# Kernel optimization log

Measured on AMD Instinct MI355X. Metric: run time of the kernel, lower is better.

The kernel has to match this reference:

```python
import jax, jax.numpy as jnp
import numpy as np
import math

D_DIM = 512
N_HEAD = 8
HIDDEN = 2048
N_LAYERS = 4
CONTEXT = 64
MAX_LEN = 5000


def make_pe(d_model, max_len=MAX_LEN):
    position = np.arange(max_len)[:, None].astype(np.float32)
    div_term = np.exp(np.arange(0, d_model, 2).astype(np.float32) * (-math.log(10000.0) / d_model))
    pe = np.zeros((max_len, d_model), dtype=np.float32)
    pe[:, 0::2] = np.sin(position * div_term)
    pe[:, 1::2] = np.cos(position * div_term)
    return jnp.asarray(pe)


def setup_inputs() -> dict:
    key = jax.random.key(0)
    ks = jax.random.split(key, 64)
    B, T, IN = 16, 2048, 512
    inp = {}
    inp["trajectory"] = jax.random.normal(ks[0], (B, T, IN), dtype=jnp.float32)
    inp["obs_length"] = jax.random.randint(ks[1], (B,), 0, T)
    s = 0.02
    inp["w_in"] = jax.random.normal(ks[2], (IN, D_DIM), dtype=jnp.float32) * s
    inp["b_in"] = jnp.zeros((D_DIM,), dtype=jnp.float32)
    # per-layer params
    params = []
    ki = 3
    for l in range(N_LAYERS):
        p = {}
        p["w_qkv"] = jax.random.normal(ks[ki], (D_DIM, 3 * D_DIM), dtype=jnp.float32) * s; ki += 1
        p["b_qkv"] = jnp.zeros((3 * D_DIM,), dtype=jnp.float32)
        p["w_o"] = jax.random.normal(ks[ki], (D_DIM, D_DIM), dtype=jnp.float32) * s; ki += 1
        p["b_o"] = jnp.zeros((D_DIM,), dtype=jnp.float32)
        p["w_ff1"] = jax.random.normal(ks[ki], (D_DIM, HIDDEN), dtype=jnp.float32) * s; ki += 1
        p["b_ff1"] = jnp.zeros((HIDDEN,), dtype=jnp.float32)
        p["w_ff2"] = jax.random.normal(ks[ki], (HIDDEN, D_DIM), dtype=jnp.float32) * s; ki += 1
        p["b_ff2"] = jnp.zeros((D_DIM,), dtype=jnp.float32)
        p["ln1_g"] = jnp.ones((D_DIM,), dtype=jnp.float32)
        p["ln1_b"] = jnp.zeros((D_DIM,), dtype=jnp.float32)
        p["ln2_g"] = jnp.ones((D_DIM,), dtype=jnp.float32)
        p["ln2_b"] = jnp.zeros((D_DIM,), dtype=jnp.float32)
        for name, v in p.items():
            inp[f"L{l}_{name}"] = v
    return inp


def layer_norm(x, g, b, eps=1e-5):
    mu = jnp.mean(x, axis=-1, keepdims=True)
    var = jnp.mean((x - mu) ** 2, axis=-1, keepdims=True)
    return (x - mu) * jax.lax.rsqrt(var + eps) * g + b


def build_attn_mask(T, obs_length, context_length):
    # boolean mask, True = masked out. Causal + per-sample context window.
    i = jnp.arange(T)[:, None]
    j = jnp.arange(T)[None, :]
    causal = j > i  # (T, T)
    # window restriction applies for rows i with context_length < i < obs_length:
    # mask positions j <= i - context_length - 1, i.e. j < i - context_length
    window = j < (i - context_length)  # (T,T)
    row_active = (i[None, :, :] > context_length) & (i[None, :, :] < obs_length[:, None, None])  # (B,T,1)
    mask = causal[None] | (window[None] & row_active)  # (B,T,T)
    return mask


def encoder_layer(x, mask_add, pad_bool, p):
    B, T, D = x.shape
    H = N_HEAD
    Dh = D // H
    qkv = x @ p["w_qkv"] + p["b_qkv"]  # (B,T,3D)
    q, k, v = jnp.split(qkv, 3, axis=-1)
    q = q.reshape(B, T, H, Dh).transpose(0, 2, 1, 3)
    k = k.reshape(B, T, H, Dh).transpose(0, 2, 1, 3)
    v = v.reshape(B, T, H, Dh).transpose(0, 2, 1, 3)
    scores = jnp.einsum("bhqd,bhkd->bhqk", q, k) / jnp.sqrt(jnp.float32(Dh))
    scores = scores + mask_add[:, None] + pad_bool[:, None, None, :] * jnp.float32(-1e9)
    attn = jax.nn.softmax(scores, axis=-1)
    ctx = jnp.einsum("bhqk,bhkd->bhqd", attn, v)
    ctx = ctx.transpose(0, 2, 1, 3).reshape(B, T, D)
    attn_out = ctx @ p["w_o"] + p["b_o"]
    x = layer_norm(x + attn_out, p["ln1_g"], p["ln1_b"])
    ff = jax.nn.relu(x @ p["w_ff1"] + p["b_ff1"]) @ p["w_ff2"] + p["b_ff2"]
    x = layer_norm(x + ff, p["ln2_g"], p["ln2_b"])
    return x


def reference(trajectory, obs_length, w_in, b_in,
              L0_w_qkv, L0_b_qkv, L0_w_o, L0_b_o, L0_w_ff1, L0_b_ff1, L0_w_ff2, L0_b_ff2, L0_ln1_g, L0_ln1_b, L0_ln2_g, L0_ln2_b,
              L1_w_qkv, L1_b_qkv, L1_w_o, L1_b_o, L1_w_ff1, L1_b_ff1, L1_w_ff2, L1_b_ff2, L1_ln1_g, L1_ln1_b, L1_ln2_g, L1_ln2_b,
              L2_w_qkv, L2_b_qkv, L2_w_o, L2_b_o, L2_w_ff1, L2_b_ff1, L2_w_ff2, L2_b_ff2, L2_ln1_g, L2_ln1_b, L2_ln2_g, L2_ln2_b,
              L3_w_qkv, L3_b_qkv, L3_w_o, L3_b_o, L3_w_ff1, L3_b_ff1, L3_w_ff2, L3_b_ff2, L3_ln1_g, L3_ln1_b, L3_ln2_g, L3_ln2_b):
    B, T, _ = trajectory.shape
    pad = jnp.arange(T)[None, :] > obs_length[:, None]  # (B,T) True = pad
    x = trajectory @ w_in + b_in
    x = x + make_pe(D_DIM)[None, :T]
    mask_bool = build_attn_mask(T, obs_length, CONTEXT)  # (B,T,T)
    mask_add = jnp.where(mask_bool, jnp.float32(-1e9), jnp.float32(0.0))
    layers = [
        dict(w_qkv=L0_w_qkv, b_qkv=L0_b_qkv, w_o=L0_w_o, b_o=L0_b_o, w_ff1=L0_w_ff1, b_ff1=L0_b_ff1, w_ff2=L0_w_ff2, b_ff2=L0_b_ff2, ln1_g=L0_ln1_g, ln1_b=L0_ln1_b, ln2_g=L0_ln2_g, ln2_b=L0_ln2_b),
        dict(w_qkv=L1_w_qkv, b_qkv=L1_b_qkv, w_o=L1_w_o, b_o=L1_b_o, w_ff1=L1_w_ff1, b_ff1=L1_b_ff1, w_ff2=L1_w_ff2, b_ff2=L1_b_ff2, ln1_g=L1_ln1_g, ln1_b=L1_ln1_b, ln2_g=L1_ln2_g, ln2_b=L1_ln2_b),
        dict(w_qkv=L2_w_qkv, b_qkv=L2_b_qkv, w_o=L2_w_o, b_o=L2_b_o, w_ff1=L2_w_ff1, b_ff1=L2_b_ff1, w_ff2=L2_w_ff2, b_ff2=L2_b_ff2, ln1_g=L2_ln1_g, ln1_b=L2_ln1_b, ln2_g=L2_ln2_g, ln2_b=L2_ln2_b),
        dict(w_qkv=L3_w_qkv, b_qkv=L3_b_qkv, w_o=L3_w_o, b_o=L3_b_o, w_ff1=L3_w_ff1, b_ff1=L3_b_ff1, w_ff2=L3_w_ff2, b_ff2=L3_b_ff2, ln1_g=L3_ln1_g, ln1_b=L3_ln1_b, ln2_g=L3_ln2_g, ln2_b=L3_ln2_b),
    ]
    for p in layers:
        x = encoder_layer(x, mask_add, pad, p)
    # aggregate
    keep = ~pad
    x = x * keep[:, :, None]
    denom = jnp.sum(keep, axis=1).astype(x.dtype)[:, None]
    return jnp.sum(x, axis=1) / denom
```

## Files before the change

### kernel.cpp

```cpp
#include <hip/hip_runtime.h>

typedef unsigned short u16;
typedef unsigned int u32;
typedef __bf16 bf16x8 __attribute__((ext_vector_type(8)));
typedef float f32x4 __attribute__((ext_vector_type(4)));

#define MFMA16(a, b, c) __builtin_amdgcn_mfma_f32_16x16x32_bf16((a), (b), (c), 0, 0, 0)

__device__ __forceinline__ u16 f2bf(float x) {
    union { float f; u32 u; } v; v.f = x;
    u32 r = v.u + 0x7fffu + ((v.u >> 16) & 1u);
    return (u16)(r >> 16);
}
__device__ __forceinline__ float bf2f(u16 x) {
    union { u32 u; float f; } v; v.u = ((u32)x) << 16; return v.f;
}

typedef const __attribute__((address_space(1))) u32* gas1_t;
typedef __attribute__((address_space(3))) u32* las3_t;
__device__ __forceinline__ void g2lds16(const void* g, void* l) {
    __builtin_amdgcn_global_load_lds((gas1_t)g, (las3_t)l, 16, 0, 0);
}

template <int MODE>
__global__ __launch_bounds__(256) void gemm_bf16(
    const u16* __restrict__ A, const u16* __restrict__ BT,
    const float* __restrict__ bias, float* __restrict__ outF,
    u16* __restrict__ outB, const float* __restrict__ aux,
    const int* __restrict__ obs,
    int M, int N, int K)
{
    __shared__ u16 As[2][128 * 32];
    __shared__ u16 Bs[2][128 * 32];
    const int tid = threadIdx.x;
    const int w = tid >> 6, l = tid & 63;
    const int gx = gridDim.x, gy = gridDim.y;
    const int orig = blockIdx.y * gx + blockIdx.x;
    int tm, tn;
    if ((gy & 15) == 0) {
        const int xcd = orig & 7;
        const int loc = orig >> 3;
        tn = loc % gx;
        const int j = loc / gx;
        const int bb = j >> 1;
        tm = bb * 16 + ((xcd - bb) & 7) + ((j & 1) << 3);
    } else {
        tm = blockIdx.y; tn = blockIdx.x;
    }
    const int bm = tm * 128, bn = tn * 128;
    if ((bm & 2047) > obs[bm >> 11]) return;
    const int wr = (w >> 1) * 64, wc = (w & 1) * 64;
    const int larow = l >> 2, lacol = (l & 3) * 8;
    f32x4 acc[4][4] = {};

    const int r0a = 16 * w, r0b = 16 * (w + 4);
    const u16* Ap = &A[(size_t)(bm + larow) * K + lacol];
    const u16* Bp = &BT[(size_t)(bn + larow) * K + lacol];

    {
        g2lds16(Ap + (size_t)r0a * K, &As[0][r0a * 32]);
        g2lds16(Bp + (size_t)r0a * K, &Bs[0][r0a * 32]);
        g2lds16(Ap + (size_t)r0b * K, &As[0][r0b * 32]);
        g2lds16(Bp + (size_t)r0b * K, &Bs[0][r0b * 32]);
    }
    __syncthreads();
    int cur = 0;
    const int nk = K >> 5;
    for (int ki = 0; ki < nk; ++ki) {
        if (ki + 1 < nk) {
            const int kt = (ki + 1) << 5;
            g2lds16(Ap + (size_t)r0a * K + kt, &As[cur ^ 1][r0a * 32]);
            g2lds16(Bp + (size_t)r0a * K + kt, &Bs[cur ^ 1][r0a * 32]);
            g2lds16(Ap + (size_t)r0b * K + kt, &As[cur ^ 1][r0b * 32]);
            g2lds16(Bp + (size_t)r0b * K + kt, &Bs[cur ^ 1][r0b * 32]);
        }
        bf16x8 af[4], bfr[4];
        #pragma unroll
        for (int i = 0; i < 4; ++i)
            af[i] = *(const bf16x8*)&As[cur][(wr + i * 16 + (l & 15)) * 32 + 8 * (l >> 4)];
        #pragma unroll
        for (int j = 0; j < 4; ++j)
            bfr[j] = *(const bf16x8*)&Bs[cur][(wc + j * 16 + (l & 15)) * 32 + 8 * (l >> 4)];
        #pragma unroll
        for (int i = 0; i < 4; ++i)
            #pragma unroll
            for (int j = 0; j < 4; ++j)
                acc[i][j] = MFMA16(af[i], bfr[j], acc[i][j]);
        __syncthreads();
        cur ^= 1;
    }

    const int r0 = bm + wr + (l >> 4) * 4;
    const int c0 = bn + wc + (l & 15);
    #pragma unroll
    for (int i = 0; i < 4; ++i) {
        #pragma unroll
        for (int j = 0; j < 4; ++j) {
            const int col = c0 + j * 16;
            const float bc = bias[col];
            #pragma unroll
            for (int r = 0; r < 4; ++r) {
                const int row = r0 + i * 16 + r;
                const size_t idx = (size_t)row * N + col;
                float val = acc[i][j][r] + bc;
                if constexpr (MODE == 0) {
                    val += aux[(size_t)(row & 2047) * 512 + col];
                    outF[idx] = val;
                    outB[idx] = f2bf(val);
                } else if constexpr (MODE == 1) {
                    outB[idx] = f2bf(val);
                } else if constexpr (MODE == 2) {
                    outF[idx] = val + aux[idx];
                } else {
                    outB[idx] = f2bf(fmaxf(val, 0.f));
                }
            }
        }
    }
}

__global__ void pe_kernel(float* __restrict__ PE) {
    const int idx = blockIdx.x * 256 + threadIdx.x;
    const int t = idx >> 8, p = idx & 255;
    const float fr = expf((float)(2 * p) * -0.017988946039015984f);
    const float arg = (float)t * fr;
    float s, c;
    sincosf(arg, &s, &c);
    float2 v = {s, c};
    *(float2*)&PE[(size_t)t * 512 + 2 * p] = v;
}

__global__ __launch_bounds__(256) void attn_kernel(
    const u16* __restrict__ QKV, u16* __restrict__ CTX, const int* __restrict__ obs,
    float* __restrict__ PBm, float* __restrict__ PBl, float* __restrict__ PBo)
{
    __shared__ u16 Ks[64 * 64];
    __shared__ u16 Vt[64 * 64];
    __shared__ u16 Ps[4][16 * 64];
    const int b = blockIdx.z, h = blockIdx.y;
    const int L = obs[b];
    const int tid = threadIdx.x, w = tid >> 6, l = tid & 63;
    const size_t tb = (size_t)b * 2048;

    if (blockIdx.x >= 32) {
        const int cbase = (blockIdx.x - 32) * 4;
        if (cbase * 64 > L) return;
        const int cc = cbase + w;
        float* pP = (float*)Ks;
        u16 q16[64];
        #pragma unroll
        for (int dd = 0; dd < 8; ++dd)
            *(uint4*)&q16[dd * 8] = *(const uint4*)&QKV[(tb + L) * 1536 + h * 64 + dd * 8];
        const int j = cc * 64 + l;
        const bool val = (j <= L);
        float s = -3.0e38f;
        if (val) {
            s = 0.f;
            const u16* kp = &QKV[(tb + j) * 1536 + 512 + h * 64];
            #pragma unroll
            for (int dd = 0; dd < 8; ++dd) {
                uint4 kk = *(const uint4*)&kp[dd * 8];
                const u16* ke = (const u16*)&kk;
                #pragma unroll
                for (int e = 0; e < 8; ++e)
                    s += bf2f(q16[dd * 8 + e]) * bf2f(ke[e]);
            }
            s *= 0.125f;
        }
        float mx = s;
        #pragma unroll
        for (int d = 1; d < 64; d <<= 1) mx = fmaxf(mx, __shfl_xor(mx, d, 64));
        const float p = val ? __expf(s - mx) : 0.f;
        float ps = p;
        #pragma unroll
        for (int d = 1; d < 64; d <<= 1) ps += __shfl_xor(ps, d, 64);
        pP[w * 64 + l] = p;
        __builtin_amdgcn_wave_barrier();
        if (cc * 64 <= L) {
            float oacc = 0.f;
            #pragma unroll 4
            for (int jj = 0; jj < 64; ++jj) {
                const int key = cc * 64 + jj;
                const int rr = (key <= L) ? key : L;
                oacc += pP[w * 64 + jj] * bf2f(QKV[(tb + rr) * 1536 + 1024 + h * 64 + l]);
            }
            const int pidx = (b * 8 + h) * 32 + cc;
            PBo[(size_t)pidx * 64 + l] = oacc;
            if (l == 0) { PBm[pidx] = mx; PBl[pidx] = ps; }
        }
        return;
    }

    const int i0 = blockIdx.x * 64;
    if (i0 > L) return;

    bf16x8 qa0, qa1;
    {
        const int qrow = i0 + 16 * w + (l & 15);
        const u16* qp = &QKV[(tb + qrow) * 1536 + h * 64];
        qa0 = *(const bf16x8*)(qp + 8 * (l >> 4));
        qa1 = *(const bf16x8*)(qp + 32 + 8 * (l >> 4));
    }
    const int g0 = (l >> 4) ^ (l & 7);
    const int g1 = ((l >> 4) + 4) ^ (l & 7);

    float m_r[4] = {-1e30f, -1e30f, -1e30f, -1e30f};
    float l_r[4] = {0.f, 0.f, 0.f, 0.f};
    f32x4 acc_o[4] = {};
    const int klo = (i0 >= 128) ? (i0 - 64) : 0;
    int khi = (L < klo) ? klo : min(i0 + 63, L);

    for (int j0 = klo; j0 <= khi; j0 += 64) {
        __syncthreads();
        {
            const int krow0 = 8 * w + (l >> 3);
            const int kswz = ((l & 7) ^ (l >> 3)) << 3;
            #pragma unroll
            for (int q = 0; q < 2; ++q) {
                const int row = krow0 + 32 * q;
                g2lds16(&QKV[(tb + j0 + row) * 1536 + 512 + h * 64 + kswz],
                        &Ks[(8 * w + 32 * q) * 64]);
            }
            const int vr = tid >> 3, c8 = (tid & 7) * 8;
            #pragma unroll
            for (int q = 0; q < 2; ++q) {
                const int row = vr + 32 * q;
                uint4 vv = *(const uint4*)&QKV[(tb + j0 + row) * 1536 + 1024 + h * 64 + c8];
                const u16* vs = (const u16*)&vv;
                #pragma unroll
                for (int e = 0; e < 8; ++e) {
                    const int d = c8 + e;
                    Vt[d * 64 + (((row >> 3) ^ e) << 3) + (row & 7)] = vs[e];
                }
            }
        }
        __syncthreads();
        f32x4 s[4];
        #pragma unroll
        for (int f = 0; f < 4; ++f) {
            f32x4 z = {0.f, 0.f, 0.f, 0.f};
            const int rowk = (f * 16 + (l & 15)) * 64;
            bf16x8 kb0 = *(const bf16x8*)&Ks[rowk + g0 * 8];
            bf16x8 kb1 = *(const bf16x8*)&Ks[rowk + g1 * 8];
            z = MFMA16(qa0, kb0, z);
            z = MFMA16(qa1, kb1, z);
            s[f] = z;
        }
        float pm[4];
        #pragma unroll
        for (int r = 0; r < 4; ++r) {
            const int i_r = i0 + 16 * w + (l >> 4) * 4 + r;
            float mx = -__builtin_inff();
            #pragma unroll
            for (int f = 0; f < 4; ++f) {
                const int j = j0 + f * 16 + (l & 15);
                float sv = s[f][r] * 0.125f;
                const bool ok = (i_r >= L) ? (j == klo)
                              : (j <= i_r && (i_r <= 64 || j >= i_r - 64));
                sv = ok ? sv : -__builtin_inff();
                s[f][r] = sv;
                mx = fmaxf(mx, sv);
            }
            pm[r] = mx;
        }
        #pragma unroll
        for (int d = 1; d < 16; d <<= 1)
            #pragma unroll
            for (int r = 0; r < 4; ++r) pm[r] = fmaxf(pm[r], __shfl_xor(pm[r], d, 64));
        float sc[4];
        #pragma unroll
        for (int r = 0; r < 4; ++r) {
            const float mn = fmaxf(m_r[r], fmaxf(pm[r], -1e30f));
            sc[r] = __expf(m_r[r] - mn);
            m_r[r] = mn;
            l_r[r] *= sc[r];
        }
        #pragma unroll
        for (int f = 0; f < 4; ++f)
            #pragma unroll
            for (int r = 0; r < 4; ++r) acc_o[f][r] *= sc[r];
        float ps[4] = {0.f, 0.f, 0.f, 0.f};
        #pragma unroll
        for (int f = 0; f < 4; ++f)
            #pragma unroll
            for (int r = 0; r < 4; ++r) {
                const float p = __expf(s[f][r] - m_r[r]);
                s[f][r] = p;
                ps[r] += p;
            }
        #pragma unroll
        for (int d = 1; d < 16; d <<= 1)
            #pragma unroll
            for (int r = 0; r < 4; ++r) ps[r] += __shfl_xor(ps[r], d, 64);
        #pragma unroll
        for (int r = 0; r < 4; ++r) l_r[r] += ps[r];
        {
            const int cg = ((l >> 3) & 1);
            #pragma unroll
            for (int f = 0; f < 4; ++f)
                #pragma unroll
                for (int r = 0; r < 4; ++r) {
                    const int prow = (l >> 4) * 4 + r;
                    Ps[w][prow * 64 + (((f * 2 + cg) ^ (prow & 7)) << 3) + (l & 7)] =
                        f2bf(s[f][r]);
                }
        }
        bf16x8 pa0 = *(const bf16x8*)&Ps[w][(l & 15) * 64 + g0 * 8];
        bf16x8 pa1 = *(const bf16x8*)&Ps[w][(l & 15) * 64 + g1 * 8];
        #pragma unroll
        for (int f = 0; f < 4; ++f) {
            const int dv = (f * 16 + (l & 15)) * 64;
            bf16x8 vb0 = *(const bf16x8*)&Vt[dv + g0 * 8];
            bf16x8 vb1 = *(const bf16x8*)&Vt[dv + g1 * 8];
            acc_o[f] = MFMA16(pa0, vb0, acc_o[f]);
            acc_o[f] = MFMA16(pa1, vb1, acc_o[f]);
        }
    }
    #pragma unroll
    for (int r = 0; r < 4; ++r) {
        const float inv = 1.f / l_r[r];
        const int row = i0 + 16 * w + (l >> 4) * 4 + r;
        if (row != L) {
            #pragma unroll
            for (int f = 0; f < 4; ++f)
                CTX[(tb + row) * 512 + h * 64 + f * 16 + (l & 15)] = f2bf(acc_o[f][r] * inv);
        }
    }
}

__global__ void attn_merge(const float* __restrict__ PBm, const float* __restrict__ PBl,
                           const float* __restrict__ PBo, u16* __restrict__ CTX,
                           const int* __restrict__ obs)
{
    const int h = blockIdx.x, b = blockIdx.y, l = threadIdx.x;
    const int L = obs[b];
    const int nc = (L >> 6) + 1;
    const int base = (b * 8 + h) * 32;
    float m = -3.0e38f;
    for (int c = 0; c < nc; ++c) m = fmaxf(m, PBm[base + c]);
    float lt = 0.f, ot = 0.f;
    for (int c = 0; c < nc; ++c) {
        const float sc = __expf(PBm[base + c] - m);
        lt += sc * PBl[base + c];
        ot += sc * PBo[(size_t)(base + c) * 64 + l];
    }
    CTX[((size_t)b * 2048 + L) * 512 + h * 64 + l] = f2bf(ot / lt);
}

__global__ __launch_bounds__(256) void ln_kernel(
    const float* __restrict__ Y, const float* __restrict__ gw,
    const float* __restrict__ bw, float* __restrict__ X, u16* __restrict__ Xb,
    const int* __restrict__ obs)
{
    const int tok0 = blockIdx.x * 4;
    if ((tok0 & 2047) > obs[tok0 >> 11]) return;
    const int tok = tok0 + (threadIdx.x >> 6);
    const int l = threadIdx.x & 63;
    const float* y = &Y[(size_t)tok * 512 + l * 8];
    f32x4 v0 = *(const f32x4*)y;
    f32x4 v1 = *(const f32x4*)(y + 4);
    float s = 0.f, sq = 0.f;
    #pragma unroll
    for (int e = 0; e < 4; ++e) {
        s += v0[e] + v1[e];
        sq += v0[e] * v0[e] + v1[e] * v1[e];
    }
    #pragma unroll
    for (int d = 1; d < 64; d <<= 1) {
        s += __shfl_xor(s, d, 64);
        sq += __shfl_xor(sq, d, 64);
    }
    const float mean = s * (1.f / 512.f);
    const float var = sq * (1.f / 512.f) - mean * mean;
    const float rstd = rsqrtf(var + 1e-5f);
    f32x4 o0, o1;
    union { u16 us[8]; uint4 u4; } pk;
    #pragma unroll
    for (int e = 0; e < 8; ++e) {
        const int d = l * 8 + e;
        const float xv = (e < 4) ? v0[e] : v1[e - 4];
        const float ov = (xv - mean) * rstd * gw[d] + bw[d];
        if (e < 4) o0[e] = ov; else o1[e - 4] = ov;
        pk.us[e] = f2bf(ov);
    }
    float* xo = &X[(size_t)tok * 512 + l * 8];
    *(f32x4*)xo = o0;
    *(f32x4*)(xo + 4) = o1;
    *(uint4*)&Xb[(size_t)tok * 512 + l * 8] = pk.u4;
}

__global__ void cast_bf16_kernel(const float* __restrict__ in, u16* __restrict__ out, int n) {
    const int i = (blockIdx.x * 256 + threadIdx.x) * 4;
    if (i + 3 < n) {
        f32x4 v = *(const f32x4*)&in[i];
        union { u16 us[4]; uint2 u2; } pk;
        #pragma unroll
        for (int e = 0; e < 4; ++e) pk.us[e] = f2bf(v[e]);
        *(uint2*)&out[i] = pk.u2;
    }
}

__global__ void transpose_cast(const float* __restrict__ W, u16* __restrict__ WT, int K, int N) {
    __shared__ float t[32][33];
    const int n0 = blockIdx.x * 32, k0 = blockIdx.y * 32;
    const int tx = threadIdx.x, ty = threadIdx.y;
    #pragma unroll
    for (int r = 0; r < 32; r += 8)
        t[ty + r][tx] = W[(size_t)(k0 + ty + r) * N + n0 + tx];
    __syncthreads();
    #pragma unroll
    for (int r = 0; r < 32; r += 8)
        WT[(size_t)(n0 + ty + r) * K + k0 + tx] = f2bf(t[tx][ty + r]);
}

struct WPack { const float* src[16]; u16* dst[16]; };
__global__ void transpose_all(WPack p) {
    __shared__ float t[32][33];
    int id = blockIdx.x;
    const int lyr = id / 3072;
    id -= lyr * 3072;
    int wi, K, N;
    if (id < 768)       { wi = 0; K = 512;  N = 1536; }
    else if (id < 1024) { wi = 1; K = 512;  N = 512;  id -= 768; }
    else if (id < 2048) { wi = 2; K = 512;  N = 2048; id -= 1024; }
    else                { wi = 3; K = 2048; N = 512;  id -= 2048; }
    const float* W = p.src[lyr * 4 + wi];
    u16* D = p.dst[lyr * 4 + wi];
    const int nx = N >> 5;
    const int n0 = (id % nx) * 32, k0 = (id / nx) * 32;
    const int tx = threadIdx.x, ty = threadIdx.y;
    #pragma unroll
    for (int r = 0; r < 32; r += 8)
        t[ty + r][tx] = W[(size_t)(k0 + ty + r) * N + n0 + tx];
    __syncthreads();
    #pragma unroll
    for (int r = 0; r < 32; r += 8)
        D[(size_t)(n0 + ty + r) * K + k0 + tx] = f2bf(t[tx][ty + r]);
}

__global__ void agg_partial(const float* __restrict__ X, float* __restrict__ part,
                            const int* __restrict__ obs) {
    const int b = blockIdx.y, c = blockIdx.x, d = threadIdx.x;
    const int L = obs[b];
    float s = 0.f;
    const int t0 = c * 128;
    int tend = t0 + 128;
    if (tend > L + 1) tend = L + 1;
    for (int t = t0; t < tend; ++t) s += X[((size_t)b * 2048 + t) * 512 + d];
    part[((size_t)b * 16 + c) * 512 + d] = s;
}

__global__ void agg_final(const float* __restrict__ part, float* __restrict__ out,
                          const int* __restrict__ obs) {
    const int b = blockIdx.x, d = threadIdx.x;
    float s = 0.f;
    #pragma unroll
    for (int c = 0; c < 16; ++c) s += part[((size_t)b * 16 + c) * 512 + d];
    out[b * 512 + d] = s / (float)(obs[b] + 1);
}

extern "C" void kernel_launch(void* const* d_in, const int* in_sizes, int n_in,
                              void* d_out, int out_size, void* d_ws, size_t ws_size,
                              hipStream_t stream)
{
    const int M = 32768;
    const int FCH = 16384;
    const float* traj = (const float*)d_in[0];
    const int* obs = (const int*)d_in[1];
    const float* w_in = (const float*)d_in[2];
    const float* b_in = (const float*)d_in[3];

    char* base = (char*)d_ws;
    size_t off = 0;
    auto carve = [&](size_t bytes) -> void* {
        void* p = base + off;
        off += (bytes + 255) & ~(size_t)255;
        return p;
    };
    u16* U     = (u16*)carve((size_t)M * 1536 * 2);
    u16* Xb    = (u16*)carve((size_t)M * 512 * 2);
    float* X   = (float*)carve((size_t)M * 512 * 4);
    float* PE  = (float*)carve((size_t)2048 * 512 * 4);
    float* PBm = (float*)carve((size_t)16 * 8 * 32 * 4);
    float* PBl = (float*)carve((size_t)16 * 8 * 32 * 4);
    float* PBo = (float*)carve((size_t)16 * 8 * 32 * 64 * 4);
    float* part = (float*)carve((size_t)16 * 16 * 512 * 4);
    u16* wTin  = (u16*)carve((size_t)512 * 512 * 2);
    u16 *wqkv[4], *wo[4], *wff1[4], *wff2[4];
    for (int l = 0; l < 4; ++l) {
        wqkv[l] = (u16*)carve((size_t)1536 * 512 * 2);
        wo[l]   = (u16*)carve((size_t)512 * 512 * 2);
        wff1[l] = (u16*)carve((size_t)2048 * 512 * 2);
        wff2[l] = (u16*)carve((size_t)512 * 2048 * 2);
    }

    dim3 tb32(32, 8);
    pe_kernel<<<2048, 256, 0, stream>>>(PE);
    transpose_cast<<<dim3(16, 16), tb32, 0, stream>>>(w_in, wTin, 512, 512);
    {
        WPack p;
        for (int l = 0; l < 4; ++l) {
            const int bi = 4 + 12 * l;
            p.src[l * 4 + 0] = (const float*)d_in[bi + 0];
            p.src[l * 4 + 1] = (const float*)d_in[bi + 2];
            p.src[l * 4 + 2] = (const float*)d_in[bi + 4];
            p.src[l * 4 + 3] = (const float*)d_in[bi + 6];
            p.dst[l * 4 + 0] = wqkv[l];
            p.dst[l * 4 + 1] = wo[l];
            p.dst[l * 4 + 2] = wff1[l];
            p.dst[l * 4 + 3] = wff2[l];
        }
        transpose_all<<<12288, tb32, 0, stream>>>(p);
    }

    cast_bf16_kernel<<<(M * 512) / 1024, 256, 0, stream>>>(traj, U, M * 512);
    gemm_bf16<0><<<dim3(4, M / 128), 256, 0, stream>>>(
        U, wTin, b_in, X, Xb, PE, obs, M, 512, 512);

    for (int lyr = 0; lyr < 4; ++lyr) {
        const int bi = 4 + 12 * lyr;
        const float* b_qkv = (const float*)d_in[bi + 1];
        const float* b_o   = (const float*)d_in[bi + 3];
        const float* b_ff1 = (const float*)d_in[bi + 5];
        const float* b_ff2 = (const float*)d_in[bi + 7];
        const float* ln1g  = (const float*)d_in[bi + 8];
        const float* ln1b  = (const float*)d_in[bi + 9];
        const float* ln2g  = (const float*)d_in[bi + 10];
        const float* ln2b  = (const float*)d_in[bi + 11];

        gemm_bf16<1><<<dim3(12, M / 128), 256, 0, stream>>>(
            Xb, wqkv[lyr], b_qkv, nullptr, U, nullptr, obs, M, 1536, 512);
        attn_kernel<<<dim3(40, 8, 16), 256, 0, stream>>>(U, Xb, obs, PBm, PBl, PBo);
        attn_merge<<<dim3(8, 16), 64, 0, stream>>>(PBm, PBl, PBo, Xb, obs);
        gemm_bf16<2><<<dim3(4, M / 128), 256, 0, stream>>>(
            Xb, wo[lyr], b_o, X, nullptr, X, obs, M, 512, 512);
        ln_kernel<<<M / 4, 256, 0, stream>>>(X, ln1g, ln1b, X, Xb, obs);
        for (int c = 0; c < 2; ++c) {
            gemm_bf16<3><<<dim3(16, FCH / 128), 256, 0, stream>>>(
                Xb + (size_t)c * FCH * 512, wff1[lyr], b_ff1, nullptr, U, nullptr,
                obs + c * 8, FCH, 2048, 512);
            gemm_bf16<2><<<dim3(4, FCH / 128), 256, 0, stream>>>(
                U, wff2[lyr], b_ff2, X + (size_t)c * FCH * 512, nullptr,
                X + (size_t)c * FCH * 512, obs + c * 8, FCH, 512, 2048);
        }
        ln_kernel<<<M / 4, 256, 0, stream>>>(X, ln2g, ln2b, X, Xb, obs);
    }

    agg_partial<<<dim3(16, 16), 512, 0, stream>>>(X, part, obs);
    agg_final<<<16, 512, 0, stream>>>(part, (float*)d_out, obs);
}
```

Baseline: 1.360 ms.

## Add BK=64 XOR-swizzled GEMM variant and unchunk FFN when workspace allows

Templates the GEMM on K-tile depth and adds a BK=64 path that stages 64-wide K slices into LDS with an XOR swizzle to avoid bank conflicts, halving the number of barrier-separated iterations. The narrow-N GEMMs (input proj, out proj, FF2) use it. When the workspace is large enough, the FFN runs over all 32768 rows in one launch pair instead of two chunks, which cuts launch count and tail effects. The cost is more LDS per block, which may lower occupancy, and the larger U buffer.

```diff
diff --git a/kernel.cpp b/kernel.cpp
--- a/kernel.cpp
+++ b/kernel.cpp
@@ -22,7 +22,7 @@
     __builtin_amdgcn_global_load_lds((gas1_t)g, (las3_t)l, 16, 0, 0);
 }
 
-template <int MODE>
+template <int MODE, int BK>
 __global__ __launch_bounds__(256) void gemm_bf16(
     const u16* __restrict__ A, const u16* __restrict__ BT,
     const float* __restrict__ bias, float* __restrict__ outF,
@@ -30,8 +30,8 @@
     const int* __restrict__ obs,
     int M, int N, int K)
 {
-    __shared__ u16 As[2][128 * 32];
-    __shared__ u16 Bs[2][128 * 32];
+    __shared__ u16 As[2][128 * BK];
+    __shared__ u16 Bs[2][128 * BK];
     const int tid = threadIdx.x;
     const int w = tid >> 6, l = tid & 63;
     const int gx = gridDim.x, gy = gridDim.y;
@@ -50,48 +50,75 @@
     const int bm = tm * 128, bn = tn * 128;
     if ((bm & 2047) > obs[bm >> 11]) return;
     const int wr = (w >> 1) * 64, wc = (w & 1) * 64;
+    f32x4 acc[4][4] = {};
+    const int lane15 = l & 15, lhi = l >> 4;
+
     const int larow = l >> 2, lacol = (l & 3) * 8;
-    f32x4 acc[4][4] = {};
-
     const int r0a = 16 * w, r0b = 16 * (w + 4);
     const u16* Ap = &A[(size_t)(bm + larow) * K + lacol];
     const u16* Bp = &BT[(size_t)(bn + larow) * K + lacol];
-
-    {
-        g2lds16(Ap + (size_t)r0a * K, &As[0][r0a * 32]);
-        g2lds16(Bp + (size_t)r0a * K, &Bs[0][r0a * 32]);
-        g2lds16(Ap + (size_t)r0b * K, &As[0][r0b * 32]);
-        g2lds16(Bp + (size_t)r0b * K, &Bs[0][r0b * 32]);
-    }
+    const int srow = l >> 3;
+    const int scol = ((l & 7) ^ srow) << 3;
+
+    auto STAGE = [&](int buf, int kt) {
+        if constexpr (BK == 32) {
+            g2lds16(Ap + (size_t)r0a * K + kt, &As[buf][r0a * 32]);
+            g2lds16(Bp + (size_t)r0a * K + kt, &Bs[buf][r0a * 32]);
+            g2lds16(Ap + (size_t)r0b * K + kt, &As[buf][r0b * 32]);
+            g2lds16(Bp + (size_t)r0b * K + kt, &Bs[buf][r0b * 32]);
+        } else {
+            #pragma unroll
+            for (int q = 0; q < 4; ++q) {
+                const int rr = w * 32 + q * 8;
+                g2lds16(&A[(size_t)(bm + rr + srow) * K + kt + scol], &As[buf][rr * 64]);
+                g2lds16(&BT[(size_t)(bn + rr + srow) * K + kt + scol], &Bs[buf][rr * 64]);
+            }
+        }
+    };
+
+    STAGE(0, 0);
     __syncthreads();
     int cur = 0;
-    const int nk = K >> 5;
+    const int nk = K / BK;
     for (int ki = 0; ki < nk; ++ki) {
-        if (ki + 1 < nk) {
-            const int kt = (ki + 1) << 5;
-            g2lds16(Ap + (size_t)r0a * K + kt, &As[cur ^ 1][r0a * 32]);
-            g2lds16(Bp + (size_t)r0a * K + kt, &Bs[cur ^ 1][r0a * 32]);
-            g2lds16(Ap + (size_t)r0b * K + kt, &As[cur ^ 1][r0b * 32]);
-            g2lds16(Bp + (size_t)r0b * K + kt, &Bs[cur ^ 1][r0b * 32]);
-        }
-        bf16x8 af[4], bfr[4];
-        #pragma unroll
-        for (int i = 0; i < 4; ++i)
-            af[i] = *(const bf16x8*)&As[cur][(wr + i * 16 + (l & 15)) * 32 + 8 * (l >> 4)];
-        #pragma unroll
-        for (int j = 0; j < 4; ++j)
-            bfr[j] = *(const bf16x8*)&Bs[cur][(wc + j * 16 + (l & 15)) * 32 + 8 * (l >> 4)];
-        #pragma unroll
-        for (int i = 0; i < 4; ++i)
+        if (ki + 1 < nk) STAGE(cur ^ 1, (ki + 1) * BK);
+        if constexpr (BK == 32) {
+            bf16x8 af[4], bfr[4];
+            #pragma unroll
+            for (int i = 0; i < 4; ++i)
+                af[i] = *(const bf16x8*)&As[cur][(wr + i * 16 + lane15) * 32 + 8 * lhi];
             #pragma unroll
             for (int j = 0; j < 4; ++j)
-                acc[i][j] = MFMA16(af[i], bfr[j], acc[i][j]);
+                bfr[j] = *(const bf16x8*)&Bs[cur][(wc + j * 16 + lane15) * 32 + 8 * lhi];
+            #pragma unroll
+            for (int i = 0; i < 4; ++i)
+                #pragma unroll
+                for (int j = 0; j < 4; ++j)
+                    acc[i][j] = MFMA16(af[i], bfr[j], acc[i][j]);
+        } else {
+            #pragma unroll
+            for (int kk = 0; kk < 2; ++kk) {
+                const int gsw = ((kk * 4 + lhi) ^ (l & 7)) << 3;
+                bf16x8 af[4], bfr[4];
+                #pragma unroll
+                for (int i = 0; i < 4; ++i)
+                    af[i] = *(const bf16x8*)&As[cur][(wr + i * 16 + lane15) * 64 + gsw];
+                #pragma unroll
+                for (int j = 0; j < 4; ++j)
+                    bfr[j] = *(const bf16x8*)&Bs[cur][(wc + j * 16 + lane15) * 64 + gsw];
+                #pragma unroll
+                for (int i = 0; i < 4; ++i)
+                    #pragma unroll
+                    for (int j = 0; j < 4; ++j)
+                        acc[i][j] = MFMA16(af[i], bfr[j], acc[i][j]);
+            }
+        }
         __syncthreads();
         cur ^= 1;
     }
 
-    const int r0 = bm + wr + (l >> 4) * 4;
-    const int c0 = bn + wc + (l & 15);
+    const int r0 = bm + wr + lhi * 4;
+    const int c0 = bn + wc + lane15;
     #pragma unroll
     for (int i = 0; i < 4; ++i) {
         #pragma unroll
@@ -465,6 +492,7 @@
 {
     const int M = 32768;
     const int FCH = 16384;
+    const bool bigws = ws_size >= (size_t)270 * 1024 * 1024;
     const float* traj = (const float*)d_in[0];
     const int* obs = (const int*)d_in[1];
     const float* w_in = (const float*)d_in[2];
@@ -477,7 +505,7 @@
         off += (bytes + 255) & ~(size_t)255;
         return p;
     };
-    u16* U     = (u16*)carve((size_t)M * 1536 * 2);
+    u16* U     = (u16*)carve((size_t)M * (bigws ? 2048 : 1536) * 2);
     u16* Xb    = (u16*)carve((size_t)M * 512 * 2);
     float* X   = (float*)carve((size_t)M * 512 * 4);
     float* PE  = (float*)carve((size_t)2048 * 512 * 4);
@@ -514,7 +542,7 @@
     }
 
     cast_bf16_kernel<<<(M * 512) / 1024, 256, 0, stream>>>(traj, U, M * 512);
-    gemm_bf16<0><<<dim3(4, M / 128), 256, 0, stream>>>(
+    gemm_bf16<0, 64><<<dim3(4, M / 128), 256, 0, stream>>>(
         U, wTin, b_in, X, Xb, PE, obs, M, 512, 512);
 
     for (int lyr = 0; lyr < 4; ++lyr) {
@@ -528,20 +556,27 @@
         const float* ln2g  = (const float*)d_in[bi + 10];
         const float* ln2b  = (const float*)d_in[bi + 11];
 
-        gemm_bf16<1><<<dim3(12, M / 128), 256, 0, stream>>>(
+        gemm_bf16<1, 32><<<dim3(12, M / 128), 256, 0, stream>>>(
             Xb, wqkv[lyr], b_qkv, nullptr, U, nullptr, obs, M, 1536, 512);
         attn_kernel<<<dim3(40, 8, 16), 256, 0, stream>>>(U, Xb, obs, PBm, PBl, PBo);
         attn_merge<<<dim3(8, 16), 64, 0, stream>>>(PBm, PBl, PBo, Xb, obs);
-        gemm_bf16<2><<<dim3(4, M / 128), 256, 0, stream>>>(
+        gemm_bf16<2, 64><<<dim3(4, M / 128), 256, 0, stream>>>(
             Xb, wo[lyr], b_o, X, nullptr, X, obs, M, 512, 512);
         ln_kernel<<<M / 4, 256, 0, stream>>>(X, ln1g, ln1b, X, Xb, obs);
-        for (int c = 0; c < 2; ++c) {
-            gemm_bf16<3><<<dim3(16, FCH / 128), 256, 0, stream>>>(
-                Xb + (size_t)c * FCH * 512, wff1[lyr], b_ff1, nullptr, U, nullptr,
-                obs + c * 8, FCH, 2048, 512);
-            gemm_bf16<2><<<dim3(4, FCH / 128), 256, 0, stream>>>(
-                U, wff2[lyr], b_ff2, X + (size_t)c * FCH * 512, nullptr,
-                X + (size_t)c * FCH * 512, obs + c * 8, FCH, 512, 2048);
+        if (bigws) {
+            gemm_bf16<3, 32><<<dim3(16, M / 128), 256, 0, stream>>>(
+                Xb, wff1[lyr], b_ff1, nullptr, U, nullptr, obs, M, 2048, 512);
+            gemm_bf16<2, 64><<<dim3(4, M / 128), 256, 0, stream>>>(
+                U, wff2[lyr], b_ff2, X, nullptr, X, obs, M, 512, 2048);
+        } else {
+            for (int c = 0; c < 2; ++c) {
+                gemm_bf16<3, 32><<<dim3(16, FCH / 128), 256, 0, stream>>>(
+                    Xb + (size_t)c * FCH * 512, wff1[lyr], b_ff1, nullptr, U, nullptr,
+                    obs + c * 8, FCH, 2048, 512);
+                gemm_bf16<2, 64><<<dim3(4, FCH / 128), 256, 0, stream>>>(
+                    U, wff2[lyr], b_ff2, X + (size_t)c * FCH * 512, nullptr,
+                    X + (size_t)c * FCH * 512, obs + c * 8, FCH, 512, 2048);
+            }
         }
         ln_kernel<<<M / 4, 256, 0, stream>>>(X, ln2g, ln2b, X, Xb, obs);
     }
```

Result: faster. 1.267 ms (-6.9%).

## Triple-buffer GEMM LDS loads with swizzle and run FFN unchunked when workspace allows

Applied to the files above, without the earlier changes.

The GEMM moves from double to triple buffering. Each iteration waits with a partial vmcnt and one barrier instead of a full syncthreads after compute, so global-to-LDS loads for two stages ahead overlap with the MFMA work. The LDS column offset is XOR-swizzled on both the write and read side to reduce bank conflicts. When the workspace is large enough, the FFN runs as one full-M pair of GEMMs instead of two chunks, which cuts launches and tail effects. In exchange, LDS use rises by half and the code depends on hand-written waitcnt counts being correct.

```diff
diff --git a/kernel.cpp b/kernel.cpp
--- a/kernel.cpp
+++ b/kernel.cpp
@@ -30,8 +30,8 @@
     const int* __restrict__ obs,
     int M, int N, int K)
 {
-    __shared__ u16 As[2][128 * 32];
-    __shared__ u16 Bs[2][128 * 32];
+    __shared__ u16 As[3][128 * 32];
+    __shared__ u16 Bs[3][128 * 32];
     const int tid = threadIdx.x;
     const int w = tid >> 6, l = tid & 63;
     const int gx = gridDim.x, gy = gridDim.y;
@@ -50,48 +50,54 @@
     const int bm = tm * 128, bn = tn * 128;
     if ((bm & 2047) > obs[bm >> 11]) return;
     const int wr = (w >> 1) * 64, wc = (w & 1) * 64;
-    const int larow = l >> 2, lacol = (l & 3) * 8;
     f32x4 acc[4][4] = {};
-
+    const int lane15 = l & 15, lhi = l >> 4;
+
+    const int larow = l >> 2;
+    const int lacol = (((l & 3) ^ ((l >> 3) & 3)) << 3);
     const int r0a = 16 * w, r0b = 16 * (w + 4);
     const u16* Ap = &A[(size_t)(bm + larow) * K + lacol];
     const u16* Bp = &BT[(size_t)(bn + larow) * K + lacol];
 
-    {
-        g2lds16(Ap + (size_t)r0a * K, &As[0][r0a * 32]);
-        g2lds16(Bp + (size_t)r0a * K, &Bs[0][r0a * 32]);
-        g2lds16(Ap + (size_t)r0b * K, &As[0][r0b * 32]);
-        g2lds16(Bp + (size_t)r0b * K, &Bs[0][r0b * 32]);
-    }
-    __syncthreads();
+    auto STAGE = [&](int buf, int kt) {
+        g2lds16(Ap + (size_t)r0a * K + kt, &As[buf][r0a * 32]);
+        g2lds16(Bp + (size_t)r0a * K + kt, &Bs[buf][r0a * 32]);
+        g2lds16(Ap + (size_t)r0b * K + kt, &As[buf][r0b * 32]);
+        g2lds16(Bp + (size_t)r0b * K + kt, &Bs[buf][r0b * 32]);
+    };
+
+    const int nk = K >> 5;
+    STAGE(0, 0);
+    STAGE(1, 32);
+    const int gsw = ((lhi ^ ((lane15 >> 1) & 3)) << 3);
     int cur = 0;
-    const int nk = K >> 5;
     for (int ki = 0; ki < nk; ++ki) {
         if (ki + 1 < nk) {
-            const int kt = (ki + 1) << 5;
-            g2lds16(Ap + (size_t)r0a * K + kt, &As[cur ^ 1][r0a * 32]);
-            g2lds16(Bp + (size_t)r0a * K + kt, &Bs[cur ^ 1][r0a * 32]);
-            g2lds16(Ap + (size_t)r0b * K + kt, &As[cur ^ 1][r0b * 32]);
-            g2lds16(Bp + (size_t)r0b * K + kt, &Bs[cur ^ 1][r0b * 32]);
+            asm volatile("s_waitcnt vmcnt(4)\n\ts_barrier" ::: "memory");
+        } else {
+            asm volatile("s_waitcnt vmcnt(0)\n\ts_barrier" ::: "memory");
+        }
+        if (ki + 2 < nk) {
+            int tgt = cur + 2; if (tgt >= 3) tgt -= 3;
+            STAGE(tgt, (ki + 2) << 5);
         }
         bf16x8 af[4], bfr[4];
         #pragma unroll
         for (int i = 0; i < 4; ++i)
-            af[i] = *(const bf16x8*)&As[cur][(wr + i * 16 + (l & 15)) * 32 + 8 * (l >> 4)];
+            af[i] = *(const bf16x8*)&As[cur][(wr + i * 16 + lane15) * 32 + gsw];
         #pragma unroll
         for (int j = 0; j < 4; ++j)
-            bfr[j] = *(const bf16x8*)&Bs[cur][(wc + j * 16 + (l & 15)) * 32 + 8 * (l >> 4)];
+            bfr[j] = *(const bf16x8*)&Bs[cur][(wc + j * 16 + lane15) * 32 + gsw];
         #pragma unroll
         for (int i = 0; i < 4; ++i)
             #pragma unroll
             for (int j = 0; j < 4; ++j)
                 acc[i][j] = MFMA16(af[i], bfr[j], acc[i][j]);
-        __syncthreads();
-        cur ^= 1;
-    }
-
-    const int r0 = bm + wr + (l >> 4) * 4;
-    const int c0 = bn + wc + (l & 15);
+        cur = (cur == 2) ? 0 : cur + 1;
+    }
+
+    const int r0 = bm + wr + lhi * 4;
+    const int c0 = bn + wc + lane15;
     #pragma unroll
     for (int i = 0; i < 4; ++i) {
         #pragma unroll
@@ -465,6 +471,7 @@
 {
     const int M = 32768;
     const int FCH = 16384;
+    const bool bigws = ws_size >= (size_t)270 * 1024 * 1024;
     const float* traj = (const float*)d_in[0];
     const int* obs = (const int*)d_in[1];
     const float* w_in = (const float*)d_in[2];
@@ -477,7 +484,7 @@
         off += (bytes + 255) & ~(size_t)255;
         return p;
     };
-    u16* U     = (u16*)carve((size_t)M * 1536 * 2);
+    u16* U     = (u16*)carve((size_t)M * (bigws ? 2048 : 1536) * 2);
     u16* Xb    = (u16*)carve((size_t)M * 512 * 2);
     float* X   = (float*)carve((size_t)M * 512 * 4);
     float* PE  = (float*)carve((size_t)2048 * 512 * 4);
@@ -535,13 +542,20 @@
         gemm_bf16<2><<<dim3(4, M / 128), 256, 0, stream>>>(
             Xb, wo[lyr], b_o, X, nullptr, X, obs, M, 512, 512);
         ln_kernel<<<M / 4, 256, 0, stream>>>(X, ln1g, ln1b, X, Xb, obs);
-        for (int c = 0; c < 2; ++c) {
-            gemm_bf16<3><<<dim3(16, FCH / 128), 256, 0, stream>>>(
-                Xb + (size_t)c * FCH * 512, wff1[lyr], b_ff1, nullptr, U, nullptr,
-                obs + c * 8, FCH, 2048, 512);
-            gemm_bf16<2><<<dim3(4, FCH / 128), 256, 0, stream>>>(
-                U, wff2[lyr], b_ff2, X + (size_t)c * FCH * 512, nullptr,
-                X + (size_t)c * FCH * 512, obs + c * 8, FCH, 512, 2048);
+        if (bigws) {
+            gemm_bf16<3><<<dim3(16, M / 128), 256, 0, stream>>>(
+                Xb, wff1[lyr], b_ff1, nullptr, U, nullptr, obs, M, 2048, 512);
+            gemm_bf16<2><<<dim3(4, M / 128), 256, 0, stream>>>(
+                U, wff2[lyr], b_ff2, X, nullptr, X, obs, M, 512, 2048);
+        } else {
+            for (int c = 0; c < 2; ++c) {
+                gemm_bf16<3><<<dim3(16, FCH / 128), 256, 0, stream>>>(
+                    Xb + (size_t)c * FCH * 512, wff1[lyr], b_ff1, nullptr, U, nullptr,
+                    obs + c * 8, FCH, 2048, 512);
+                gemm_bf16<2><<<dim3(4, FCH / 128), 256, 0, stream>>>(
+                    U, wff2[lyr], b_ff2, X + (size_t)c * FCH * 512, nullptr,
+                    X + (size_t)c * FCH * 512, obs + c * 8, FCH, 512, 2048);
+            }
         }
         ln_kernel<<<M / 4, 256, 0, stream>>>(X, ln2g, ln2b, X, Xb, obs);
     }
```

New measurement: 1.345 ms. Within noise of the previous version (-1.1%).
